# Performance work log

Measured on AMD Instinct MI355X. Metric: run time of the kernel, lower is better.

## Reference

```python
import jax, jax.numpy as jnp
import numpy as np

MAX_NODES = 32767   # complete binary tree, depth 15 (2**15 - 1)
N_FEATURES = 256
N_ACTIONS = 64
BATCH = 262144


def _build_tree(key):
    """Valid complete binary tree: internal node i has children 2i+1, 2i+2; leaves -1/-1."""
    idx = np.arange(MAX_NODES)
    left = 2 * idx + 1
    right = 2 * idx + 2
    internal = right < MAX_NODES
    children_left = np.where(internal, left, -1).astype(np.int32)
    children_right = np.where(internal, right, -1).astype(np.int32)
    k1, k2 = jax.random.split(key)
    features = jax.random.randint(k1, (MAX_NODES,), 0, N_FEATURES, dtype=jnp.int32)
    thresholds = jax.random.normal(k2, (MAX_NODES,), dtype=jnp.float32)
    return features, thresholds, jnp.asarray(children_left), jnp.asarray(children_right)


def setup_inputs() -> dict:
    key = jax.random.key(0)
    k_obs, k_tree, k_leaf = jax.random.split(key, 3)
    features, thresholds, children_left, children_right = _build_tree(k_tree)
    obs = jax.random.normal(k_obs, (BATCH, N_FEATURES), dtype=jnp.float32)
    leaf_logits = jax.random.normal(k_leaf, (MAX_NODES, N_ACTIONS), dtype=jnp.float32)
    return {
        "obs": obs,
        "features": features,
        "thresholds": thresholds,
        "children_left": children_left,
        "children_right": children_right,
        "leaf_logits": leaf_logits,
    }


def reference(obs, features, thresholds, children_left, children_right, leaf_logits):
    # Faithful translation of the flax module's while_loop tree traversal,
    # vmapped over a batch of observations.
    def traverse(o):  # o: [n_features]
        def cond(node_id):
            return children_left[node_id] != children_right[node_id]

        def body(node_id):
            go_left = o[features[node_id]] <= thresholds[node_id]
            return jax.lax.select(go_left, children_left[node_id], children_right[node_id])

        return jax.lax.while_loop(cond, body, jnp.int32(0))

    leaf_ids = jax.vmap(traverse)(obs)          # [B] int32
    return leaf_logits[leaf_ids]                # [B, n_actions]
```

## Files before the change

kernel.cpp:

```cpp
#include <hip/hip_runtime.h>


#define N_INTERN  16383
#define N_FEAT    256
#define N_ACT     64
#define BATCH     262144
#define BLOCK     512
#define GRID      256
#define ROWS_PB   (BATCH / GRID)
#define HROWS     32
#define HALVES    (ROWS_PB / HROWS)
#define DEPTH     14
#define PFN       4
#define TSLOTS    (HROWS * N_FEAT / 4)

typedef float f32x4 __attribute__((ext_vector_type(4)));

__global__ __launch_bounds__(BLOCK, 1) void tree_policy_kernel(
    const float* __restrict__ obs,
    const int*   __restrict__ features,
    const float* __restrict__ thresholds,
    const float* __restrict__ leaf_logits,
    float*       __restrict__ out)
{
    __shared__ float         sthr [N_INTERN];
    __shared__ unsigned char sfeat[N_INTERN];
    __shared__ __align__(16) f32x4 buf[2][TSLOTS];

    const int tid  = threadIdx.x;
    const int lane = tid & 63;
    const int wave = tid >> 6;
    const long rowBase = (long)blockIdx.x * ROWS_PB;
    const f32x4* gsrc = (const f32x4*)(obs + rowBase * N_FEAT);

    for (int i = tid; i < N_INTERN; i += BLOCK) {
        sthr[i]  = thresholds[i];
        sfeat[i] = (unsigned char)features[i];
    }
    const float thr_root  = thresholds[0];
    const int   feat_root = features[0];

    f32x4 pfA[PFN], pfB[PFN];
#pragma unroll
    for (int k = 0; k < PFN; ++k)
        pfA[k] = __builtin_nontemporal_load(&gsrc[0 * TSLOTS + k * BLOCK + tid]);
#pragma unroll
    for (int k = 0; k < PFN; ++k)
        pfB[k] = __builtin_nontemporal_load(&gsrc[1 * TSLOTS + k * BLOCK + tid]);

    asm volatile("s_waitcnt lgkmcnt(0)" ::: "memory");
    __builtin_amdgcn_s_barrier();

    const int myrow_id = (wave << 2) | (lane >> 4);
    const int chunk    = lane & 15;

    auto half_body = [&](int h, f32x4 (&pf)[PFN]) {
        const int b = h & 1;
        if (h == 0)                 asm volatile("s_waitcnt vmcnt(4)" ::: "memory");
        else if (h == HALVES - 1)   asm volatile("s_waitcnt vmcnt(2)" ::: "memory");
        else                        asm volatile("s_waitcnt vmcnt(6)" ::: "memory");
        __builtin_amdgcn_sched_barrier(0);
#pragma unroll
        for (int k = 0; k < PFN; ++k)
            buf[b][k * BLOCK + tid] = pf[k];
        if (h + 2 < HALVES) {
#pragma unroll
            for (int k = 0; k < PFN; ++k)
                pf[k] = __builtin_nontemporal_load(
                    &gsrc[(long)(h + 2) * TSLOTS + k * BLOCK + tid]);
        }
        asm volatile("s_waitcnt lgkmcnt(0)" ::: "memory");
        __builtin_amdgcn_s_barrier();
        __builtin_amdgcn_sched_barrier(0);

        const float* myrow = (const float*)&buf[b][0] + myrow_id * N_FEAT;
        int   node = 0;
        float tcur = thr_root;
        int   fcur = feat_root;
#pragma unroll
        for (int d = 0; d < DEPTH - 1; ++d) {
            const float x   = myrow[fcur];
            const int   c   = 2 * node + 1;
            const float tl  = sthr[c];
            const float trr = sthr[c + 1];
            const int   fl  = sfeat[c];
            const int   fr  = sfeat[c + 1];
            const bool  L   = (x <= tcur);
            node = L ? c : c + 1;
            tcur = L ? tl : trr;
            fcur = L ? fl : fr;
        }
        {
            const float x = myrow[fcur];
            node = 2 * node + ((x <= tcur) ? 1 : 2);
        }

        const long orow = rowBase + (long)h * HROWS + myrow_id;
        const f32x4 v = *(const f32x4*)(leaf_logits + (size_t)node * N_ACT + chunk * 4);
        __builtin_nontemporal_store(v, (f32x4*)(out + orow * N_ACT + chunk * 4));
    };

    for (int hh = 0; hh < HALVES; hh += 2) {
        half_body(hh,     pfA);
        half_body(hh + 1, pfB);
    }
}

extern "C" void kernel_launch(void* const* d_in, const int* in_sizes, int n_in,
                              void* d_out, int out_size, void* d_ws, size_t ws_size,
                              hipStream_t stream) {
    const float* obs         = (const float*)d_in[0];
    const int*   features    = (const int*)  d_in[1];
    const float* thresholds  = (const float*)d_in[2];
    const float* leaf_logits = (const float*)d_in[5];
    float*       out         = (float*)d_out;

    tree_policy_kernel<<<dim3(GRID), dim3(BLOCK), 0, stream>>>(
        obs, features, thresholds, leaf_logits, out);
}
```

Baseline: 64.54 us.

## Pack child thresholds and features in pairs and pad obs rows in LDS

Thresholds and feature ids of sibling children are stored together, as a float2 and a packed ushort indexed by parent. Each traversal step then needs two LDS loads instead of four. The staged observation rows are padded to a stride of 65 float4s so that the 16 rows read by a wave spread across different LDS banks. The cost is slightly more LDS and extra index arithmetic when staging rows.

```diff
diff --git a/kernel.cpp b/kernel.cpp
--- a/kernel.cpp
+++ b/kernel.cpp
@@ -1,7 +1,7 @@
 #include <hip/hip_runtime.h>
 
 
-#define N_INTERN  16383
+#define N_PAIR    8191
 #define N_FEAT    256
 #define N_ACT     64
 #define BATCH     262144
@@ -12,7 +12,8 @@
 #define HALVES    (ROWS_PB / HROWS)
 #define DEPTH     14
 #define PFN       4
-#define TSLOTS    (HROWS * N_FEAT / 4)
+#define RSTRIDE4  65
+#define TSLOTS    (HROWS * RSTRIDE4)
 
 typedef float f32x4 __attribute__((ext_vector_type(4)));
 
@@ -23,8 +24,8 @@
     const float* __restrict__ leaf_logits,
     float*       __restrict__ out)
 {
-    __shared__ float         sthr [N_INTERN];
-    __shared__ unsigned char sfeat[N_INTERN];
+    __shared__ float2         sthr2 [N_PAIR];
+    __shared__ unsigned short sfeat2[N_PAIR];
     __shared__ __align__(16) f32x4 buf[2][TSLOTS];
 
     const int tid  = threadIdx.x;
@@ -33,9 +34,10 @@
     const long rowBase = (long)blockIdx.x * ROWS_PB;
     const f32x4* gsrc = (const f32x4*)(obs + rowBase * N_FEAT);
 
-    for (int i = tid; i < N_INTERN; i += BLOCK) {
-        sthr[i]  = thresholds[i];
-        sfeat[i] = (unsigned char)features[i];
+    for (int i = tid; i < N_PAIR; i += BLOCK) {
+        sthr2[i]  = make_float2(thresholds[2 * i + 1], thresholds[2 * i + 2]);
+        sfeat2[i] = (unsigned short)((features[2 * i + 1] & 255) |
+                                     ((features[2 * i + 2] & 255) << 8));
     }
     const float thr_root  = thresholds[0];
     const int   feat_root = features[0];
@@ -43,10 +45,10 @@
     f32x4 pfA[PFN], pfB[PFN];
 #pragma unroll
     for (int k = 0; k < PFN; ++k)
-        pfA[k] = __builtin_nontemporal_load(&gsrc[0 * TSLOTS + k * BLOCK + tid]);
+        pfA[k] = __builtin_nontemporal_load(&gsrc[0 * (HROWS * N_FEAT / 4) + k * BLOCK + tid]);
 #pragma unroll
     for (int k = 0; k < PFN; ++k)
-        pfB[k] = __builtin_nontemporal_load(&gsrc[1 * TSLOTS + k * BLOCK + tid]);
+        pfB[k] = __builtin_nontemporal_load(&gsrc[1 * (HROWS * N_FEAT / 4) + k * BLOCK + tid]);
 
     asm volatile("s_waitcnt lgkmcnt(0)" ::: "memory");
     __builtin_amdgcn_s_barrier();
@@ -61,34 +63,33 @@
         else                        asm volatile("s_waitcnt vmcnt(6)" ::: "memory");
         __builtin_amdgcn_sched_barrier(0);
 #pragma unroll
-        for (int k = 0; k < PFN; ++k)
-            buf[b][k * BLOCK + tid] = pf[k];
+        for (int k = 0; k < PFN; ++k) {
+            const int s = k * BLOCK + tid;
+            buf[b][(s >> 6) * RSTRIDE4 + (s & 63)] = pf[k];
+        }
         if (h + 2 < HALVES) {
 #pragma unroll
             for (int k = 0; k < PFN; ++k)
                 pf[k] = __builtin_nontemporal_load(
-                    &gsrc[(long)(h + 2) * TSLOTS + k * BLOCK + tid]);
+                    &gsrc[(long)(h + 2) * (HROWS * N_FEAT / 4) + k * BLOCK + tid]);
         }
         asm volatile("s_waitcnt lgkmcnt(0)" ::: "memory");
         __builtin_amdgcn_s_barrier();
         __builtin_amdgcn_sched_barrier(0);
 
-        const float* myrow = (const float*)&buf[b][0] + myrow_id * N_FEAT;
+        const float* myrow = (const float*)&buf[b][0] + myrow_id * (RSTRIDE4 * 4);
         int   node = 0;
         float tcur = thr_root;
         int   fcur = feat_root;
 #pragma unroll
         for (int d = 0; d < DEPTH - 1; ++d) {
-            const float x   = myrow[fcur];
-            const int   c   = 2 * node + 1;
-            const float tl  = sthr[c];
-            const float trr = sthr[c + 1];
-            const int   fl  = sfeat[c];
-            const int   fr  = sfeat[c + 1];
-            const bool  L   = (x <= tcur);
-            node = L ? c : c + 1;
-            tcur = L ? tl : trr;
-            fcur = L ? fl : fr;
+            const float    x   = myrow[fcur];
+            const float2   tch = sthr2[node];
+            const unsigned fp  = sfeat2[node];
+            const bool L = (x <= tcur);
+            node = 2 * node + (L ? 1 : 2);
+            tcur = L ? tch.x : tch.y;
+            fcur = (int)(L ? (fp & 255u) : (fp >> 8));
         }
         {
             const float x = myrow[fcur];
```

New measurement: 66.19 us. 2.6% more time.

## Stream obs rows straight into LDS per wave and drop block barriers

Applied to the files above, without the earlier changes.

Replaces register staging of observation tiles (global load into registers, then LDS store, then block barrier) with direct global-to-LDS loads. Each wave loads only the four rows it later traverses, so synchronisation is reduced to per-wave vmcnt waits and the per-tile block barriers go away. The leaf-logit gather and output store for the previous tile are software-pipelined around the next DMA issue and the current traversal. The cost is reliance on precise vmcnt accounting and per-wave ownership of the LDS rows, which is fragile if the ordering assumptions break.

```diff
diff --git a/kernel.cpp b/kernel.cpp
--- a/kernel.cpp
+++ b/kernel.cpp
@@ -11,10 +11,14 @@
 #define HROWS     32
 #define HALVES    (ROWS_PB / HROWS)
 #define DEPTH     14
-#define PFN       4
-#define TSLOTS    (HROWS * N_FEAT / 4)
 
 typedef float f32x4 __attribute__((ext_vector_type(4)));
+typedef __attribute__((address_space(3))) void        lds_void_t;
+typedef const __attribute__((address_space(1))) void  glob_cvoid_t;
+
+__device__ __forceinline__ void gload16(const void* g, void* l) {
+    __builtin_amdgcn_global_load_lds((glob_cvoid_t*)g, (lds_void_t*)l, 16, 0, 0);
+}
 
 __global__ __launch_bounds__(BLOCK, 1) void tree_policy_kernel(
     const float* __restrict__ obs,
@@ -25,13 +29,12 @@
 {
     __shared__ float         sthr [N_INTERN];
     __shared__ unsigned char sfeat[N_INTERN];
-    __shared__ __align__(16) f32x4 buf[2][TSLOTS];
+    __shared__ __align__(16) float buf[2][HROWS * N_FEAT];
 
     const int tid  = threadIdx.x;
     const int lane = tid & 63;
     const int wave = tid >> 6;
     const long rowBase = (long)blockIdx.x * ROWS_PB;
-    const f32x4* gsrc = (const f32x4*)(obs + rowBase * N_FEAT);
 
     for (int i = tid; i < N_INTERN; i += BLOCK) {
         sthr[i]  = thresholds[i];
@@ -40,43 +43,20 @@
     const float thr_root  = thresholds[0];
     const int   feat_root = features[0];
 
-    f32x4 pfA[PFN], pfB[PFN];
-#pragma unroll
-    for (int k = 0; k < PFN; ++k)
-        pfA[k] = __builtin_nontemporal_load(&gsrc[0 * TSLOTS + k * BLOCK + tid]);
-#pragma unroll
-    for (int k = 0; k < PFN; ++k)
-        pfB[k] = __builtin_nontemporal_load(&gsrc[1 * TSLOTS + k * BLOCK + tid]);
-
-    asm volatile("s_waitcnt lgkmcnt(0)" ::: "memory");
-    __builtin_amdgcn_s_barrier();
-
     const int myrow_id = (wave << 2) | (lane >> 4);
     const int chunk    = lane & 15;
 
-    auto half_body = [&](int h, f32x4 (&pf)[PFN]) {
-        const int b = h & 1;
-        if (h == 0)                 asm volatile("s_waitcnt vmcnt(4)" ::: "memory");
-        else if (h == HALVES - 1)   asm volatile("s_waitcnt vmcnt(2)" ::: "memory");
-        else                        asm volatile("s_waitcnt vmcnt(6)" ::: "memory");
-        __builtin_amdgcn_sched_barrier(0);
+    auto dma = [&](int h) {
+        const float* g = obs + (rowBase + (long)h * HROWS + (wave << 2)) * N_FEAT + lane * 4;
+        char* l = (char*)&buf[h & 1][(wave << 2) * N_FEAT];
 #pragma unroll
-        for (int k = 0; k < PFN; ++k)
-            buf[b][k * BLOCK + tid] = pf[k];
-        if (h + 2 < HALVES) {
-#pragma unroll
-            for (int k = 0; k < PFN; ++k)
-                pf[k] = __builtin_nontemporal_load(
-                    &gsrc[(long)(h + 2) * TSLOTS + k * BLOCK + tid]);
-        }
-        asm volatile("s_waitcnt lgkmcnt(0)" ::: "memory");
-        __builtin_amdgcn_s_barrier();
-        __builtin_amdgcn_sched_barrier(0);
+        for (int k = 0; k < 4; ++k)
+            gload16(g + k * N_FEAT, l + k * 1024);
+    };
 
-        const float* myrow = (const float*)&buf[b][0] + myrow_id * N_FEAT;
-        int   node = 0;
-        float tcur = thr_root;
-        int   fcur = feat_root;
+    auto traverse = [&](int h) -> int {
+        const float* myrow = &buf[h & 1][myrow_id * N_FEAT];
+        int node = 0; float tcur = thr_root; int fcur = feat_root;
 #pragma unroll
         for (int d = 0; d < DEPTH - 1; ++d) {
             const float x   = myrow[fcur];
@@ -90,20 +70,37 @@
             tcur = L ? tl : trr;
             fcur = L ? fl : fr;
         }
-        {
-            const float x = myrow[fcur];
-            node = 2 * node + ((x <= tcur) ? 1 : 2);
-        }
-
-        const long orow = rowBase + (long)h * HROWS + myrow_id;
-        const f32x4 v = *(const f32x4*)(leaf_logits + (size_t)node * N_ACT + chunk * 4);
-        __builtin_nontemporal_store(v, (f32x4*)(out + orow * N_ACT + chunk * 4));
+        const float x = myrow[fcur];
+        return 2 * node + ((x <= tcur) ? 1 : 2);
     };
 
-    for (int hh = 0; hh < HALVES; hh += 2) {
-        half_body(hh,     pfA);
-        half_body(hh + 1, pfB);
+    dma(0);
+    asm volatile("s_waitcnt vmcnt(0) lgkmcnt(0)" ::: "memory");
+    __builtin_amdgcn_s_barrier();
+
+    dma(1);
+    __builtin_amdgcn_sched_barrier(0);
+    int node_prev = traverse(0);
+
+    for (int h = 1; h < HALVES; ++h) {
+        if (h == 1) asm volatile("s_waitcnt vmcnt(0)" ::: "memory");
+        else        asm volatile("s_waitcnt vmcnt(1)" ::: "memory");
+        __builtin_amdgcn_sched_barrier(0);
+        const f32x4 v = *(const f32x4*)(leaf_logits + (size_t)node_prev * N_ACT + chunk * 4);
+        __builtin_amdgcn_sched_barrier(0);
+        if (h + 1 < HALVES) {
+            dma(h + 1);
+            __builtin_amdgcn_sched_barrier(0);
+        }
+        const long orow = rowBase + (long)(h - 1) * HROWS + myrow_id;
+        __builtin_nontemporal_store(v, (f32x4*)(out + orow * N_ACT + chunk * 4));
+        __builtin_amdgcn_sched_barrier(0);
+        node_prev = traverse(h);
     }
+
+    const f32x4 v = *(const f32x4*)(leaf_logits + (size_t)node_prev * N_ACT + chunk * 4);
+    const long orow = rowBase + (long)(HALVES - 1) * HROWS + myrow_id;
+    __builtin_nontemporal_store(v, (f32x4*)(out + orow * N_ACT + chunk * 4));
 }
 
 extern "C" void kernel_launch(void* const* d_in, const int* in_sizes, int n_in,
```

Result: faster. 62.44 us (-3.2%).
